# Kernel optimization log

Measured on AMD Instinct MI355X. Metric: run time of the kernel, lower is better.

The kernel has to match this reference:

```python
import jax, jax.numpy as jnp
import numpy as np

B = 8192
N_COLS = 64
D = 1024
EPS = 1e-5


def _layernorm(x, g, b):
    m = jnp.mean(x, axis=-1, keepdims=True)
    v = jnp.mean(jnp.square(x - m), axis=-1, keepdims=True)
    return (x - m) * jax.lax.rsqrt(v + EPS) * g + b


def setup_inputs() -> dict:
    key = jax.random.key(0)
    ks = jax.random.split(key, 8)
    s = 0.02
    return {
        "x1_enc": jax.random.normal(ks[0], (1, N_COLS, D), jnp.float32),
        "x2_enc": jax.random.normal(ks[1], (B, D), jnp.float32),
        "We": jax.random.normal(ks[2], (4, 2 * D, D), jnp.float32) * s,
        "be": jnp.zeros((4, D), jnp.float32),
        "W1": jax.random.normal(ks[3], (2 * D, 4 * D), jnp.float32) * s,
        "b1": jnp.zeros((4 * D,), jnp.float32),
        "g1": jnp.ones((4 * D,), jnp.float32),
        "bt1": jnp.zeros((4 * D,), jnp.float32),
        "W2": jax.random.normal(ks[4], (4 * D, 2 * D), jnp.float32) * s,
        "b2": jnp.zeros((2 * D,), jnp.float32),
        "g2": jnp.ones((2 * D,), jnp.float32),
        "bt2": jnp.zeros((2 * D,), jnp.float32),
        "W3": jax.random.normal(ks[5], (2 * D, 1), jnp.float32) * s,
        "b3": jnp.zeros((1,), jnp.float32),
        "col_pairs": jax.random.randint(ks[6], (B, 2), 0, N_COLS, jnp.int64),
        "vis_type": jax.random.randint(ks[7], (B,), 0, 4, jnp.int64),
    }


def reference(x1_enc, x2_enc, We, be, W1, b1, g1, bt1, W2, b2, g2, bt2, W3, b3,
              col_pairs, vis_type):
    # x1 repeated B times is identical per row -> gather directly from x1_enc[0]
    x11 = x1_enc[0, col_pairs[:, 0]]          # [B, D]
    x12 = x1_enc[0, col_pairs[:, 1]]          # [B, D]
    x1c = jnp.concatenate([x11, x12], axis=1)  # [B, 2D]

    # 1-of-4 expert routing: compute all experts, select by vis_type
    all_y = jax.nn.relu(jnp.einsum('bd,edk->bek', x1c, We) + be)  # [B, 4, D]
    y1 = jnp.take_along_axis(all_y, vis_type[:, None, None], axis=1)[:, 0]  # [B, D]

    y = jnp.concatenate([y1, x2_enc], axis=1)  # [B, 2D]
    h = _layernorm(jax.nn.relu(y @ W1 + b1), g1, bt1)
    h = _layernorm(jax.nn.relu(h @ W2 + b2), g2, bt2)
    return jax.nn.sigmoid(h @ W3 + b3)  # [B, 1]
```

## Files before the change

kernel.cpp:

```cpp
#include <hip/hip_runtime.h>

typedef unsigned short u16;
typedef __bf16 bf16x8 __attribute__((ext_vector_type(8)));
typedef float f32x4v __attribute__((ext_vector_type(4)));
typedef u16 u16x8 __attribute__((ext_vector_type(8)));

__device__ __forceinline__ u16 f2bf(float f) {
  union { float f; unsigned u; } v; v.f = f;
  unsigned r = v.u + 0x7fffu + ((v.u >> 16) & 1u);
  return (u16)(r >> 16);
}
__device__ __forceinline__ float bf2f(u16 h) {
  union { unsigned u; float f; } v; v.u = ((unsigned)h) << 16;
  return v.f;
}

#define G2L16(g, l)                                                            \
  __builtin_amdgcn_global_load_lds((__attribute__((address_space(1))) void*)(g), \
                                   (__attribute__((address_space(3))) void*)(l), 16, 0, 0)

__global__ __launch_bounds__(256) void k_transpose2(const float* __restrict__ W1,
                                                    u16* __restrict__ W1T,
                                                    const float* __restrict__ W2,
                                                    u16* __restrict__ W2gT,
                                                    const float* __restrict__ g1,
                                                    const float* __restrict__ bt1,
                                                    float* __restrict__ w2ps,
                                                    float* __restrict__ w2pc) {
  __shared__ float tile[64][65];
  int bid = blockIdx.x;
  const float* in;
  u16* out;
  int R, C, bx, by, fold;
  if (bid < 2048) {
    in = W1; out = W1T; R = 2048; C = 4096; fold = 0;
    bx = bid & 63; by = bid >> 6;
  } else {
    bid -= 2048;
    in = W2; out = W2gT; R = 4096; C = 2048; fold = 1;
    bx = bid & 31; by = bid >> 5;
  }
  const int c0 = bx * 64, r0 = by * 64;
  const int t = threadIdx.x;
  const int tc = (t & 15) * 4, tr = t >> 4;
#pragma unroll
  for (int i = 0; i < 4; ++i) {
    int r = tr + i * 16;
    f32x4v v = *(const f32x4v*)(in + (size_t)(r0 + r) * C + c0 + tc);
    tile[r][tc] = v[0]; tile[r][tc + 1] = v[1];
    tile[r][tc + 2] = v[2]; tile[r][tc + 3] = v[3];
  }
  __syncthreads();
  const int oc = t >> 2;
  const int rb = (t & 3) * 16;
  float gv[16];
#pragma unroll
  for (int i = 0; i < 16; ++i) gv[i] = fold ? g1[r0 + rb + i] : 1.f;
  u16x8 o0, o1;
#pragma unroll
  for (int i = 0; i < 8; ++i) o0[i] = f2bf(tile[rb + i][oc] * gv[i]);
#pragma unroll
  for (int i = 0; i < 8; ++i) o1[i] = f2bf(tile[rb + 8 + i][oc] * gv[8 + i]);
  *(u16x8*)(out + (size_t)(c0 + oc) * R + r0 + rb) = o0;
  *(u16x8*)(out + (size_t)(c0 + oc) * R + r0 + rb + 8) = o1;
  if (fold) {
    float ps = 0.f, pc = 0.f;
#pragma unroll
    for (int i = 0; i < 16; ++i) {
      float w = tile[rb + i][oc];
      ps += gv[i] * w;
      pc += bt1[r0 + rb + i] * w;
    }
    ps += __shfl_down(ps, 2, 4); ps += __shfl_down(ps, 1, 4);
    pc += __shfl_down(pc, 2, 4); pc += __shfl_down(pc, 1, 4);
    if ((t & 3) == 0) {
      w2ps[(size_t)by * 2048 + c0 + oc] = ps;
      w2pc[(size_t)by * 2048 + c0 + oc] = pc;
    }
  }
}

__global__ __launch_bounds__(256) void k_pq(const float* __restrict__ x1,
                                            const float* __restrict__ We,
                                            float* __restrict__ pq0,
                                            float* __restrict__ pq1) {
  const int n0 = blockIdx.x * 64;
  const int ep = blockIdx.y;
  const int e = ep >> 1, p = ep & 1;
  const int khalf = blockIdx.z & 1;
  const int chalf = blockIdx.z >> 1;
  const int ks = khalf * 512;
  float* pq = khalf ? pq1 : pq0;
  __shared__ float As[32][33];
  __shared__ float Bs[32][68];
  const int t = threadIdx.x;
  const int tx = t & 15, ty = t >> 4;
  float acc[2][4] = {};
  const float* wbase = We + (size_t)e * 2048 * 1024 + (size_t)p * 1024 * 1024;
  for (int k0 = ks; k0 < ks + 512; k0 += 32) {
#pragma unroll
    for (int i = 0; i < 4; ++i) {
      int ix = t + i * 256;
      As[ix >> 5][ix & 31] =
          x1[(size_t)(chalf * 32 + (ix >> 5)) * 1024 + k0 + (ix & 31)];
    }
#pragma unroll
    for (int i = 0; i < 8; ++i) {
      int ix = t + i * 256;
      Bs[ix >> 6][ix & 63] = wbase[(size_t)(k0 + (ix >> 6)) * 1024 + n0 + (ix & 63)];
    }
    __syncthreads();
#pragma unroll
    for (int kk = 0; kk < 32; ++kk) {
      float av[2];
#pragma unroll
      for (int i = 0; i < 2; ++i) av[i] = As[ty * 2 + i][kk];
      f32x4v bv = *(const f32x4v*)&Bs[kk][tx * 4];
#pragma unroll
      for (int i = 0; i < 2; ++i)
#pragma unroll
        for (int j = 0; j < 4; ++j) acc[i][j] += av[i] * bv[j];
    }
    __syncthreads();
  }
#pragma unroll
  for (int i = 0; i < 2; ++i) {
    float* dst = pq + ((size_t)ep * 64 + chalf * 32 + ty * 2 + i) * 1024 + n0 + tx * 4;
#pragma unroll
    for (int j = 0; j < 4; ++j) dst[j] = acc[i][j];
  }
}

__global__ __launch_bounds__(256) void k_build_y(const float* __restrict__ pq0,
                                                 const float* __restrict__ pq1,
                                                 const float* __restrict__ x2,
                                                 const float* __restrict__ be,
                                                 const int* __restrict__ cp,
                                                 const int* __restrict__ vis,
                                                 u16* __restrict__ Y) {
  const int t = threadIdx.x;
  for (int rr = 0; rr < 8; ++rr) {
    const int b = blockIdx.x * 8 + rr;
    const int e = vis[b];
    u16x8 o;
    if (t < 128) {
      const int c0 = cp[2 * b], c1 = cp[2 * b + 1];
      const size_t po = ((size_t)(e * 2) * 64 + c0) * 1024 + t * 8;
      const size_t qo = ((size_t)(e * 2 + 1) * 64 + c1) * 1024 + t * 8;
      const float* B = be + e * 1024 + t * 8;
#pragma unroll
      for (int i = 0; i < 8; ++i) {
        float v = pq0[po + i] + pq1[po + i] + pq0[qo + i] + pq1[qo + i] + B[i];
        o[i] = f2bf(v > 0.f ? v : 0.f);
      }
      *(u16x8*)(Y + (size_t)b * 2048 + t * 8) = o;
    } else {
      const float* X = x2 + (size_t)b * 1024 + (size_t)(t - 128) * 8;
#pragma unroll
      for (int i = 0; i < 8; ++i) o[i] = f2bf(X[i]);
      *(u16x8*)(Y + (size_t)b * 2048 + 1024 + (size_t)(t - 128) * 8) = o;
    }
  }
}

template <int MODE>
__global__ __launch_bounds__(256, 3) void k_gemm(const u16* __restrict__ A,
                                                 const u16* __restrict__ BT,
                                                 const float* __restrict__ bias,
                                                 const float2* __restrict__ stats,
                                                 const float* __restrict__ s1,
                                                 const float* __restrict__ c1b,
                                                 const float* __restrict__ gw3,
                                                 float2* __restrict__ sp_out,
                                                 float4* __restrict__ part,
                                                 u16* __restrict__ C,
                                                 int M, int N, int K) {
  __shared__ u16 As[128 * 64];
  __shared__ u16 Bs[128 * 64];
  const int tid = threadIdx.x;
  const int lane = tid & 63;
  const int wave = tid >> 6;

  const int nx = gridDim.x, ny = gridDim.y;
  const int bid = blockIdx.y * nx + blockIdx.x;
  const int stripe = ny >> 3;
  const int xcd = bid & 7;
  const int loc = bid >> 3;
  const int panel = loc / (stripe * 4);
  const int rem = loc - panel * (stripe * 4);
  const int by = xcd * stripe + (rem >> 2);
  const int bx = panel * 4 + (rem & 3);
  const int tileN = bx * 128;
  const int tileM = by * 128;
  const int wm = wave & 1;
  const int wn = wave >> 1;

  f32x4v acc[4][4];
#pragma unroll
  for (int i = 0; i < 4; ++i)
#pragma unroll
    for (int j = 0; j < 4; ++j) acc[i][j] = (f32x4v){0.f, 0.f, 0.f, 0.f};

  const int srow = tid >> 3;
  const int lchunk = (tid & 7) ^ (srow & 7);
  const u16* aptr = A + (size_t)(tileM + srow) * K + lchunk * 8;
  const u16* bptr = BT + (size_t)(tileN + srow) * K + lchunk * 8;
  u16* asp = As + tid * 8;
  u16* bsp = Bs + tid * 8;

  const int s = lane & 7;
  const int kp0 = ((lane >> 4) ^ s) * 8;
  const int kp1 = kp0 ^ 32;
  const int am = wm * 64 + (lane & 15);
  const int bn = wn * 64 + (lane & 15);

  for (int k0 = 0; k0 < K; k0 += 64) {
    G2L16(aptr, asp);
    G2L16(aptr + (size_t)32 * K, asp + 2048);
    G2L16(aptr + (size_t)64 * K, asp + 4096);
    G2L16(aptr + (size_t)96 * K, asp + 6144);
    G2L16(bptr, bsp);
    G2L16(bptr + (size_t)32 * K, bsp + 2048);
    G2L16(bptr + (size_t)64 * K, bsp + 4096);
    G2L16(bptr + (size_t)96 * K, bsp + 6144);
    aptr += 64;
    bptr += 64;
    __syncthreads();

    bf16x8 af[4], bfr[4];
#pragma unroll
    for (int mi = 0; mi < 4; ++mi)
      af[mi] = *(const bf16x8*)(As + (am + mi * 16) * 64 + kp0);
#pragma unroll
    for (int ni = 0; ni < 4; ++ni)
      bfr[ni] = *(const bf16x8*)(Bs + (bn + ni * 16) * 64 + kp0);
#pragma unroll
    for (int mi = 0; mi < 4; ++mi)
#pragma unroll
      for (int ni = 0; ni < 4; ++ni)
        acc[mi][ni] = __builtin_amdgcn_mfma_f32_16x16x32_bf16(af[mi], bfr[ni], acc[mi][ni], 0, 0, 0);
#pragma unroll
    for (int mi = 0; mi < 4; ++mi)
      af[mi] = *(const bf16x8*)(As + (am + mi * 16) * 64 + kp1);
#pragma unroll
    for (int ni = 0; ni < 4; ++ni)
      bfr[ni] = *(const bf16x8*)(Bs + (bn + ni * 16) * 64 + kp1);
#pragma unroll
    for (int mi = 0; mi < 4; ++mi)
#pragma unroll
      for (int ni = 0; ni < 4; ++ni)
        acc[mi][ni] = __builtin_amdgcn_mfma_f32_16x16x32_bf16(af[mi], bfr[ni], acc[mi][ni], 0, 0, 0);
    __syncthreads();
  }

  const int crow = tileM + wm * 64 + (lane >> 4) * 4;
  const int ccol = tileN + wn * 64 + (lane & 15);
  float cv0[4], cv1[4], cg[4];
#pragma unroll
  for (int ni = 0; ni < 4; ++ni) {
    const int c = ccol + ni * 16;
    if (MODE == 0) {
      cv0[ni] = bias[c];
    } else {
      cv0[ni] = s1[c];
      cv1[ni] = c1b[c];
      cg[ni] = gw3[c];
    }
  }
  const int cb = bx * 2 + wn;
#pragma unroll
  for (int mi = 0; mi < 4; ++mi) {
#pragma unroll
    for (int r = 0; r < 4; ++r) {
      const int row = crow + mi * 16 + r;
      if (MODE == 0) {
        float s_ = 0.f, ss_ = 0.f;
#pragma unroll
        for (int ni = 0; ni < 4; ++ni) {
          float v = acc[mi][ni][r] + cv0[ni];
          v = v > 0.f ? v : 0.f;
          s_ += v; ss_ += v * v;
          C[(size_t)row * N + ccol + ni * 16] = f2bf(v);
        }
#pragma unroll
        for (int off = 8; off >= 1; off >>= 1) {
          s_ += __shfl_xor(s_, off, 16);
          ss_ += __shfl_xor(ss_, off, 16);
        }
        if ((lane & 15) == 0)
          sp_out[(size_t)row * 64 + cb] = make_float2(s_, ss_);
      } else {
        float2 st = stats[row];
        const float m = st.x, rs = st.y;
        float s_ = 0.f, ss_ = 0.f, d_ = 0.f;
#pragma unroll
        for (int ni = 0; ni < 4; ++ni) {
          float v = rs * acc[mi][ni][r] - rs * m * cv0[ni] + cv1[ni];
          v = v > 0.f ? v : 0.f;
          s_ += v; ss_ += v * v; d_ += v * cg[ni];
        }
#pragma unroll
        for (int off = 8; off >= 1; off >>= 1) {
          s_ += __shfl_xor(s_, off, 16);
          ss_ += __shfl_xor(ss_, off, 16);
          d_ += __shfl_xor(d_, off, 16);
        }
        if ((lane & 15) == 0)
          part[(size_t)row * 32 + cb] = make_float4(s_, ss_, d_, 0.f);
      }
    }
  }
}

__global__ __launch_bounds__(256) void k_reduce(const float2* __restrict__ sp,
                                                float2* __restrict__ stats,
                                                const float* __restrict__ w2ps,
                                                const float* __restrict__ w2pc,
                                                const float* __restrict__ b2,
                                                float* __restrict__ s1,
                                                float* __restrict__ c1b,
                                                const float* __restrict__ g2,
                                                const float* __restrict__ bt2,
                                                const float* __restrict__ W3,
                                                float* __restrict__ gw3,
                                                float* __restrict__ scal) {
  __shared__ float red[8];
  const int bid = blockIdx.x;
  const int t = threadIdx.x;
  if (bid < 32) {
    const int g = t >> 4, l = t & 15;
#pragma unroll 1
    for (int rr = 0; rr < 16; ++rr) {
      const int row = bid * 256 + rr * 16 + g;
      float s = 0.f, ss = 0.f;
#pragma unroll
      for (int i = 0; i < 4; ++i) {
        float2 p = sp[(size_t)row * 64 + l * 4 + i];
        s += p.x; ss += p.y;
      }
#pragma unroll
      for (int off = 8; off >= 1; off >>= 1) {
        s += __shfl_xor(s, off, 16);
        ss += __shfl_xor(ss, off, 16);
      }
      if (l == 0) {
        float m = s * (1.f / 4096.f);
        float var = ss * (1.f / 4096.f) - m * m;
        stats[row] = make_float2(m, rsqrtf(var + 1e-5f));
      }
    }
  } else if (bid < 40) {
    const int nn = (bid - 32) * 256 + t;
    float s = 0.f, c = 0.f;
    for (int kb = 0; kb < 64; ++kb) {
      s += w2ps[(size_t)kb * 2048 + nn];
      c += w2pc[(size_t)kb * 2048 + nn];
    }
    s1[nn] = s;
    c1b[nn] = c + b2[nn];
  } else {
    float sg = 0.f, cb = 0.f;
    for (int i = 0; i < 8; ++i) {
      int c = i * 256 + t;
      float w3 = W3[c];
      float gv = g2[c] * w3;
      gw3[c] = gv;
      sg += gv;
      cb += bt2[c] * w3;
    }
#pragma unroll
    for (int off = 32; off > 0; off >>= 1) {
      sg += __shfl_down(sg, off, 64);
      cb += __shfl_down(cb, off, 64);
    }
    const int lane = t & 63, wv = t >> 6;
    if (lane == 0) { red[wv] = sg; red[4 + wv] = cb; }
    __syncthreads();
    if (t == 0) {
      scal[0] = red[0] + red[1] + red[2] + red[3];
      scal[1] = red[4] + red[5] + red[6] + red[7];
    }
  }
}

__global__ __launch_bounds__(256) void k_final(const float4* __restrict__ part,
                                               const float* __restrict__ scal,
                                               const float* __restrict__ b3,
                                               float* __restrict__ out) {
  const int t = threadIdx.x;
  const int g = t >> 4, l = t & 15;
  const int row = blockIdx.x * 16 + g;
  float4 a = part[(size_t)row * 32 + l * 2];
  float4 b = part[(size_t)row * 32 + l * 2 + 1];
  float S = a.x + b.x, SS = a.y + b.y, D = a.z + b.z;
#pragma unroll
  for (int off = 8; off >= 1; off >>= 1) {
    S += __shfl_xor(S, off, 16);
    SS += __shfl_xor(SS, off, 16);
    D += __shfl_xor(D, off, 16);
  }
  if (l == 0) {
    float m = S * (1.f / 2048.f);
    float rs = rsqrtf(SS * (1.f / 2048.f) - m * m + 1e-5f);
    float logit = rs * D - rs * m * scal[0] + scal[1] + b3[0];
    out[row] = 1.f / (1.f + expf(-logit));
  }
}

extern "C" void kernel_launch(void* const* d_in, const int* in_sizes, int n_in,
                              void* d_out, int out_size, void* d_ws, size_t ws_size,
                              hipStream_t stream) {
  const float* x1 = (const float*)d_in[0];
  const float* x2 = (const float*)d_in[1];
  const float* We = (const float*)d_in[2];
  const float* be = (const float*)d_in[3];
  const float* W1 = (const float*)d_in[4];
  const float* b1 = (const float*)d_in[5];
  const float* g1 = (const float*)d_in[6];
  const float* bt1 = (const float*)d_in[7];
  const float* W2 = (const float*)d_in[8];
  const float* b2 = (const float*)d_in[9];
  const float* g2 = (const float*)d_in[10];
  const float* bt2 = (const float*)d_in[11];
  const float* W3 = (const float*)d_in[12];
  const float* b3 = (const float*)d_in[13];
  const int* cp = (const int*)d_in[14];
  const int* vis = (const int*)d_in[15];
  float* out = (float*)d_out;

  char* ws = (char*)d_ws;
  u16* W1T  = (u16*)(ws);
  u16* W2gT = (u16*)(ws + 16777216);
  u16* Y    = (u16*)(ws + 33554432);
  u16* H1   = (u16*)(ws + 67108864);
  float* PQ0 = (float*)(ws + 134217728);
  float* PQ1 = (float*)(ws + 136314880);
  float2* sp = (float2*)(ws + 134217728);
  float4* part = (float4*)(ws + 134217728);
  float2* stats = (float2*)(ws + 138412032);
  float* s1   = (float*)(ws + 138477568);
  float* c1b  = (float*)(ws + 138485760);
  float* w2ps = (float*)(ws + 138493952);
  float* w2pc = (float*)(ws + 139018240);
  float* gw3  = (float*)(ws + 139542528);
  float* scal = (float*)(ws + 139550720);

  k_transpose2<<<4096, 256, 0, stream>>>(W1, W1T, W2, W2gT, g1, bt1, w2ps, w2pc);
  k_pq<<<dim3(16, 8, 4), 256, 0, stream>>>(x1, We, PQ0, PQ1);
  k_build_y<<<1024, 256, 0, stream>>>(PQ0, PQ1, x2, be, cp, vis, Y);
  k_gemm<0><<<dim3(32, 64), 256, 0, stream>>>(
      Y, W1T, b1, nullptr, nullptr, nullptr, nullptr, sp, nullptr, H1,
      8192, 4096, 2048);
  k_reduce<<<41, 256, 0, stream>>>(sp, stats, w2ps, w2pc, b2, s1, c1b,
                                   g2, bt2, W3, gw3, scal);
  k_gemm<1><<<dim3(16, 64), 256, 0, stream>>>(
      H1, W2gT, nullptr, stats, s1, c1b, gw3, nullptr, part, nullptr,
      8192, 2048, 4096);
  k_final<<<512, 256, 0, stream>>>(part, scal, b3, out);
}
```

Before: 474.8 us.

## Register-prefetch next K tile instead of direct global-to-LDS loads in GEMM

Swaps the direct global_load_lds path for ordinary vector loads into registers, which are then written to LDS. The next K tile's global loads are issued right after the LDS store barrier, so they overlap with the MFMA work on the current tile. This hides global memory latency that the old load-then-sync loop exposed. It costs extra VGPRs for the staging registers and extra LDS store instructions, which may lower occupancy.

```diff
diff --git a/kernel.cpp b/kernel.cpp
--- a/kernel.cpp
+++ b/kernel.cpp
@@ -14,10 +14,6 @@
   union { unsigned u; float f; } v; v.u = ((unsigned)h) << 16;
   return v.f;
 }
-
-#define G2L16(g, l)                                                            \
-  __builtin_amdgcn_global_load_lds((__attribute__((address_space(1))) void*)(g), \
-                                   (__attribute__((address_space(3))) void*)(l), 16, 0, 0)
 
 __global__ __launch_bounds__(256) void k_transpose2(const float* __restrict__ W1,
                                                     u16* __restrict__ W1T,
@@ -214,18 +210,34 @@
   const int am = wm * 64 + (lane & 15);
   const int bn = wn * 64 + (lane & 15);
 
-  for (int k0 = 0; k0 < K; k0 += 64) {
-    G2L16(aptr, asp);
-    G2L16(aptr + (size_t)32 * K, asp + 2048);
-    G2L16(aptr + (size_t)64 * K, asp + 4096);
-    G2L16(aptr + (size_t)96 * K, asp + 6144);
-    G2L16(bptr, bsp);
-    G2L16(bptr + (size_t)32 * K, bsp + 2048);
-    G2L16(bptr + (size_t)64 * K, bsp + 4096);
-    G2L16(bptr + (size_t)96 * K, bsp + 6144);
-    aptr += 64;
-    bptr += 64;
+  u16x8 ra0, ra1, ra2, ra3, rb0, rb1, rb2, rb3;
+#define GLOAD                                                                  \
+  {                                                                            \
+    ra0 = *(const u16x8*)aptr;                                                 \
+    ra1 = *(const u16x8*)(aptr + (size_t)32 * K);                              \
+    ra2 = *(const u16x8*)(aptr + (size_t)64 * K);                              \
+    ra3 = *(const u16x8*)(aptr + (size_t)96 * K);                              \
+    rb0 = *(const u16x8*)bptr;                                                 \
+    rb1 = *(const u16x8*)(bptr + (size_t)32 * K);                              \
+    rb2 = *(const u16x8*)(bptr + (size_t)64 * K);                              \
+    rb3 = *(const u16x8*)(bptr + (size_t)96 * K);                              \
+    aptr += 64; bptr += 64;                                                    \
+  }
+
+  const int niter = K >> 6;
+  GLOAD;
+  for (int it = 0; it < niter; ++it) {
     __syncthreads();
+    *(u16x8*)asp = ra0;
+    *(u16x8*)(asp + 2048) = ra1;
+    *(u16x8*)(asp + 4096) = ra2;
+    *(u16x8*)(asp + 6144) = ra3;
+    *(u16x8*)bsp = rb0;
+    *(u16x8*)(bsp + 2048) = rb1;
+    *(u16x8*)(bsp + 4096) = rb2;
+    *(u16x8*)(bsp + 6144) = rb3;
+    __syncthreads();
+    if (it + 1 < niter) GLOAD;
 
     bf16x8 af[4], bfr[4];
 #pragma unroll
@@ -250,8 +262,8 @@
 #pragma unroll
       for (int ni = 0; ni < 4; ++ni)
         acc[mi][ni] = __builtin_amdgcn_mfma_f32_16x16x32_bf16(af[mi], bfr[ni], acc[mi][ni], 0, 0, 0);
-    __syncthreads();
-  }
+  }
+#undef GLOAD
 
   const int crow = tileM + wm * 64 + (lane >> 4) * 4;
   const int ccol = tileN + wn * 64 + (lane & 15);
```

After: 516.0 us. +8.7%, slower.
